# Kernel optimization log

Hardware: AMD Instinct MI355X
Metric: run time of the kernel (lower is better)

Reference implementation:

```python
import math
import jax, jax.numpy as jnp
import numpy as np

D_MODEL = 768
N_HEADS = 12
D_K = 64
D_V = 64
LN_EPS = 1e-5


def setup_inputs() -> dict:
    key = jax.random.key(0)
    ks = jax.random.split(key, 12)
    B, S = 4, 2048
    Q = jax.random.normal(ks[0], (B, S, D_MODEL), dtype=jnp.float32)
    K = jax.random.normal(ks[1], (B, S, D_MODEL), dtype=jnp.float32)
    V = jax.random.normal(ks[2], (B, S, D_MODEL), dtype=jnp.float32)
    attn_mask = jax.random.randint(ks[3], (B, S, S), 0, 2).astype(bool)
    sc = 1.0 / math.sqrt(D_MODEL)
    WQ = jax.random.normal(ks[4], (D_MODEL, N_HEADS * D_K), dtype=jnp.float32) * sc
    WK = jax.random.normal(ks[5], (D_MODEL, N_HEADS * D_K), dtype=jnp.float32) * sc
    WV = jax.random.normal(ks[6], (D_MODEL, N_HEADS * D_V), dtype=jnp.float32) * sc
    Wfc = jax.random.normal(ks[7], (N_HEADS * D_V, D_MODEL), dtype=jnp.float32) * sc
    bQ = jnp.zeros((N_HEADS * D_K,), jnp.float32)
    bK = jnp.zeros((N_HEADS * D_K,), jnp.float32)
    bV = jnp.zeros((N_HEADS * D_V,), jnp.float32)
    bfc = jnp.zeros((D_MODEL,), jnp.float32)
    gamma = jnp.ones((D_MODEL,), jnp.float32)
    beta = jnp.zeros((D_MODEL,), jnp.float32)
    return {"Q": Q, "K": K, "V": V, "attn_mask": attn_mask,
            "WQ": WQ, "bQ": bQ, "WK": WK, "bK": bK, "WV": WV, "bV": bV,
            "Wfc": Wfc, "bfc": bfc, "gamma": gamma, "beta": beta}


def reference(Q, K, V, attn_mask, WQ, bQ, WK, bK, WV, bV, Wfc, bfc, gamma, beta):
    B, S, _ = Q.shape
    # projections -> [B, H, S, d]
    q = (Q @ WQ + bQ).reshape(B, S, N_HEADS, D_K).transpose(0, 2, 1, 3)
    k = (K @ WK + bK).reshape(B, S, N_HEADS, D_K).transpose(0, 2, 1, 3)
    v = (V @ WV + bV).reshape(B, S, N_HEADS, D_V).transpose(0, 2, 1, 3)
    # manual scaled dot-product attention with masked_fill(-1e9)
    scores = jnp.einsum('bhqd,bhkd->bhqk', q, k) / math.sqrt(D_K)
    scores = jnp.where(attn_mask[:, None, :, :], jnp.float32(-1e9), scores)
    attn = jax.nn.softmax(scores, axis=-1)
    context = jnp.einsum('bhqk,bhkd->bhqd', attn, v)
    context = context.transpose(0, 2, 1, 3).reshape(B, S, N_HEADS * D_V)
    out = context @ Wfc + bfc + Q  # residual is Q
    # LayerNorm over d_model
    mu = jnp.mean(out, axis=-1, keepdims=True)
    var = jnp.mean((out - mu) ** 2, axis=-1, keepdims=True)
    return (out - mu) * jax.lax.rsqrt(var + LN_EPS) * gamma + beta
```

## Files before the change

### kernel.cpp

```cpp
#include <hip/hip_runtime.h>
#include <stdint.h>

#define DM   768
#define HEADS 12
#define DK    64
#define SEQ  2048
#define BATCH  4

typedef __bf16 bf16_t;
typedef __bf16 bf16x8 __attribute__((ext_vector_type(8)));
typedef __bf16 bf16x4 __attribute__((ext_vector_type(4)));
typedef float  f32x4  __attribute__((ext_vector_type(4)));
typedef float  f32x16 __attribute__((ext_vector_type(16)));
typedef unsigned u32x4 __attribute__((ext_vector_type(4)));

#define LOG2E 1.44269504f
#define MASKVAL (-1.442695e9f)

#define OFF_FLAG 0
#define OFF_MASK 256
#define SZ_MASK  (BATCH*SEQ*(SEQ/32)*4)
#define OFF_WT   (OFF_MASK + SZ_MASK)
#define SZ_WT1   (DM*DM*2)
#define OFF_XB   (OFF_WT + 4*SZ_WT1)
#define SZ_X     (BATCH*SEQ*DM*2)
#define OFF_QP   (OFF_XB + 3*SZ_X)
#define SZ_PROJ  (BATCH*HEADS*SEQ*DK*2)
#define OFF_KP   (OFF_QP + SZ_PROJ)
#define OFF_VT   (OFF_KP + SZ_PROJ)

__device__ __forceinline__ void gload_lds16(const bf16_t* g, bf16_t* l) {
    __builtin_amdgcn_global_load_lds((const __attribute__((address_space(1))) unsigned int*)g,
                                     (__attribute__((address_space(3))) unsigned int*)l, 16, 0, 0);
}

__device__ __forceinline__ unsigned pack2(float lo, float hi) {
    union { bf16_t b[2]; unsigned u; } x;
    x.b[0] = (bf16_t)lo; x.b[1] = (bf16_t)hi;
    return x.u;
}

__global__ void detect_mask_kernel(const unsigned char* __restrict__ m, int* flag) {
    int u = threadIdx.x;
    int any = m[4*u+1] | m[4*u+2] | m[4*u+3];
    unsigned long long b = __ballot(any != 0);
    if (u == 0) *flag = (b == 0ULL) ? 1 : 0;
}

__global__ void pack_mask_kernel(const void* __restrict__ mraw, const int* __restrict__ flag,
                                 unsigned int* __restrict__ words) {
    const unsigned int total = BATCH*SEQ*SEQ;
    const int is32 = *flag;
    const int* mi = (const int*)mraw;
    const unsigned char* mb = (const unsigned char*)mraw;
    unsigned int stride = gridDim.x * blockDim.x;
    unsigned int lane = threadIdx.x & 63u;
    for (unsigned int e = blockIdx.x * blockDim.x + threadIdx.x; e < total; e += stride) {
        int v = is32 ? (mi[e] != 0) : (mb[e] != 0);
        unsigned long long bal = __ballot(v);
        if ((lane & 31u) == 0u)
            words[e >> 5] = (unsigned int)(bal >> ((lane >> 5) * 32u));
    }
}

__global__ void wt_cvt_kernel(const float* __restrict__ W0, const float* __restrict__ W1,
                              const float* __restrict__ W2, const float* __restrict__ W3,
                              bf16_t* __restrict__ dst) {
    const float* W = blockIdx.z == 0 ? W0 : blockIdx.z == 1 ? W1 : blockIdx.z == 2 ? W2 : W3;
    bf16_t* out = dst + (size_t)blockIdx.z * DM * DM;
    __shared__ float tile[64][65];
    int w = threadIdx.x >> 6, u = threadIdx.x & 63;
    int kb = blockIdx.x * 64, nb = blockIdx.y * 64;
    #pragma unroll
    for (int i = 0; i < 16; i++)
        tile[w + 4*i][u] = W[(size_t)(kb + w + 4*i)*DM + nb + u];
    __syncthreads();
    #pragma unroll
    for (int i = 0; i < 16; i++)
        out[(size_t)(nb + w + 4*i)*DM + kb + u] = (bf16_t)tile[u][w + 4*i];
}

__global__ void xcvt_kernel(const float* __restrict__ Q, const float* __restrict__ K,
                            const float* __restrict__ V, bf16_t* __restrict__ XB) {
    int z = blockIdx.y;
    const float* src = z == 0 ? Q : z == 1 ? K : V;
    bf16_t* dst = XB + (size_t)z * BATCH*SEQ*DM;
    size_t i = ((size_t)blockIdx.x * blockDim.x + threadIdx.x) * 8;
    float4 a = *(const float4*)(src + i);
    float4 b = *(const float4*)(src + i + 4);
    bf16x8 o;
    o[0]=(bf16_t)a.x; o[1]=(bf16_t)a.y; o[2]=(bf16_t)a.z; o[3]=(bf16_t)a.w;
    o[4]=(bf16_t)b.x; o[5]=(bf16_t)b.y; o[6]=(bf16_t)b.z; o[7]=(bf16_t)b.w;
    *(bf16x8*)(dst + i) = o;
}

__device__ __forceinline__ void mm_mainloop(const bf16_t* __restrict__ Aptr,
                                            const bf16_t* __restrict__ Bptr,
                                            bf16_t* As, bf16_t* Bs,
                                            f32x4 acc[4][4], int bm, int bn) {
    int tid = threadIdx.x, w = tid >> 6, u = tid & 63, c = u & 15, g = u >> 4;
    int wr = w >> 1, wc = w & 1;
    for (int k0 = 0; k0 < DM; k0 += 64) {
        #pragma unroll
        for (int i = 0; i < 4; i++) {
            int q = i*256 + tid;
            int row = q >> 3, col8 = q & 7;
            gload_lds16(Aptr + (size_t)(bm*128 + row)*DM + k0 + col8*8, As + (i*256 + w*64)*8);
            gload_lds16(Bptr + (size_t)(bn*128 + row)*DM + k0 + col8*8, Bs + (i*256 + w*64)*8);
        }
        __syncthreads();
        #pragma unroll
        for (int kk = 0; kk < 2; kk++) {
            bf16x8 a[4], bfr[4];
            #pragma unroll
            for (int mi = 0; mi < 4; mi++)
                a[mi] = *(const bf16x8*)(As + (wr*64 + mi*16 + c)*64 + kk*32 + g*8);
            #pragma unroll
            for (int ni = 0; ni < 4; ni++)
                bfr[ni] = *(const bf16x8*)(Bs + (wc*64 + ni*16 + c)*64 + kk*32 + g*8);
            #pragma unroll
            for (int mi = 0; mi < 4; mi++)
                #pragma unroll
                for (int ni = 0; ni < 4; ni++)
                    acc[mi][ni] = __builtin_amdgcn_mfma_f32_16x16x32_bf16(a[mi], bfr[ni], acc[mi][ni], 0, 0, 0);
        }
        __syncthreads();
    }
}

__global__ __launch_bounds__(256) void proj128_kernel(
        const bf16_t* __restrict__ XB, const bf16_t* __restrict__ WT,
        const float* __restrict__ bQ, const float* __restrict__ bK, const float* __restrict__ bV,
        bf16_t* __restrict__ QP, bf16_t* __restrict__ KP, bf16_t* __restrict__ VT) {
    int z = blockIdx.z;
    const bf16_t* Aptr = XB + (size_t)z * BATCH*SEQ*DM;
    const bf16_t* Bptr = WT + (size_t)z * DM * DM;
    const float* bias = z == 0 ? bQ : z == 1 ? bK : bV;
    float scale = (z == 0) ? 0.125f * LOG2E : 1.0f;
    __shared__ __align__(16) bf16_t As[128*64], Bs[128*64];
    int tid = threadIdx.x, w = tid >> 6, u = tid & 63, c = u & 15, g = u >> 4;
    int wr = w >> 1, wc = w & 1;
    int bm = blockIdx.x, bn = blockIdx.y;
    f32x4 zero = {0.f,0.f,0.f,0.f};
    f32x4 acc[4][4] = {{zero,zero,zero,zero},{zero,zero,zero,zero},
                       {zero,zero,zero,zero},{zero,zero,zero,zero}};
    mm_mainloop(Aptr, Bptr, As, Bs, acc, bm, bn);
    int h = bn*2 + wc;
    #pragma unroll
    for (int ni = 0; ni < 4; ni++) {
        int d = ni*16 + c;
        float bv = bias[h*64 + d];
        if (z < 2) {
            bf16_t* dst = (z == 0) ? QP : KP;
            #pragma unroll
            for (int mi = 0; mi < 4; mi++)
                #pragma unroll
                for (int j = 0; j < 4; j++) {
                    int r = bm*128 + wr*64 + mi*16 + 4*g + j;
                    int bidx = r >> 11, s = r & 2047;
                    dst[(((size_t)bidx*HEADS + h)*SEQ + s)*DK + d] = (bf16_t)((acc[mi][ni][j] + bv)*scale);
                }
        } else {
            #pragma unroll
            for (int mi = 0; mi < 4; mi++) {
                bf16x4 pk;
                #pragma unroll
                for (int j = 0; j < 4; j++) pk[j] = (bf16_t)(acc[mi][ni][j] + bv);
                int r0 = bm*128 + wr*64 + mi*16 + 4*g;
                int bidx = r0 >> 11, s0 = r0 & 2047;
                *(bf16x4*)(VT + (((size_t)bidx*HEADS + h)*DK + d)*SEQ + s0) = pk;
            }
        }
    }
}

__global__ __launch_bounds__(256) void out128_kernel(
        const bf16_t* __restrict__ CTX, const bf16_t* __restrict__ WfcT,
        const float* __restrict__ bfc, const float* __restrict__ Qres, float* __restrict__ out) {
    __shared__ __align__(16) bf16_t As[128*64], Bs[128*64];
    int tid = threadIdx.x, w = tid >> 6, u = tid & 63, c = u & 15, g = u >> 4;
    int wr = w >> 1, wc = w & 1;
    int bm = blockIdx.x, bn = blockIdx.y;
    f32x4 zero = {0.f,0.f,0.f,0.f};
    f32x4 acc[4][4] = {{zero,zero,zero,zero},{zero,zero,zero,zero},
                       {zero,zero,zero,zero},{zero,zero,zero,zero}};
    mm_mainloop(CTX, WfcT, As, Bs, acc, bm, bn);
    #pragma unroll
    for (int ni = 0; ni < 4; ni++) {
        int n = bn*128 + wc*64 + ni*16 + c;
        float bv = bfc[n];
        #pragma unroll
        for (int mi = 0; mi < 4; mi++)
            #pragma unroll
            for (int j = 0; j < 4; j++) {
                int r = bm*128 + wr*64 + mi*16 + 4*g + j;
                out[(size_t)r*DM + n] = acc[mi][ni][j] + bv + Qres[(size_t)r*DM + n];
            }
    }
}

__global__ __launch_bounds__(256) void attn_kernel(
        const bf16_t* __restrict__ QP, const bf16_t* __restrict__ KP, const bf16_t* __restrict__ VT,
        const unsigned int* __restrict__ maskw, bf16_t* __restrict__ CTX) {
    __shared__ __align__(16) bf16_t kbuf[2][64*64];
    __shared__ __align__(16) bf16_t vbuf[2][64*64];
    int tid = threadIdx.x, w = tid >> 6, u = tid & 63;
    int qc = u & 31, hi = u >> 5;
    int b = blockIdx.z, h = blockIdx.y;
    int qg = blockIdx.x * 128 + w * 32 + qc;
    size_t bh = (size_t)(b * HEADS + h);
    const bf16_t* qp = QP + bh * SEQ * DK;
    const bf16_t* kp = KP + bh * SEQ * DK;
    const bf16_t* vt = VT + bh * DK * SEQ;
    const unsigned int* mwq = maskw + ((size_t)b * SEQ + qg) * (SEQ/32);

    bf16x8 qf[4];
    #pragma unroll
    for (int t = 0; t < 4; t++)
        qf[t] = *(const bf16x8*)(qp + (size_t)qg*DK + 16*t + 8*hi);

    int sr = tid >> 3, scc = tid & 7;

    f32x16 zz = {0,0,0,0,0,0,0,0,0,0,0,0,0,0,0,0};
    f32x16 acc0 = zz, acc1 = zz;
    float mrun = -3e38f, lsum = 0.f;

    #pragma unroll
    for (int i = 0; i < 2; i++) {
        int r = i*32 + sr;
        int gc = (scc ^ (r & 7)) << 3;
        gload_lds16(kp + (size_t)r*DK + gc,       &kbuf[0][0] + i*2048 + tid*8);
        gload_lds16(vt + (size_t)r*SEQ + 0 + gc,  &vbuf[0][0] + i*2048 + tid*8);
    }
    __syncthreads();

    for (int kt = 0; kt < SEQ/64; kt++) {
        int kb = kt * 64;
        int cur = kt & 1;
        if (kt + 1 < SEQ/64) {
            int nkb = kb + 64;
            #pragma unroll
            for (int i = 0; i < 2; i++) {
                int r = i*32 + sr;
                int gc = (scc ^ (r & 7)) << 3;
                gload_lds16(kp + (size_t)(nkb + r)*DK + gc, &kbuf[cur^1][0] + i*2048 + tid*8);
                gload_lds16(vt + (size_t)r*SEQ + nkb + gc,  &vbuf[cur^1][0] + i*2048 + tid*8);
            }
        }
        const bf16_t* kl = &kbuf[cur][0];
        const bf16_t* vl = &vbuf[cur][0];
        uint2 mv = *(const uint2*)(mwq + (kb >> 5));

        f32x16 s0 = zz, s1 = zz;
        __builtin_amdgcn_s_setprio(1);
        #pragma unroll
        for (int t = 0; t < 4; t++) {
            int col = (16*t + 8*hi);
            int r0 = qc, r1 = 32 + qc;
            bf16x8 k0 = *(const bf16x8*)(kl + r0*64 + (col ^ ((r0 & 7) << 3)));
            bf16x8 k1 = *(const bf16x8*)(kl + r1*64 + (col ^ ((r1 & 7) << 3)));
            s0 = __builtin_amdgcn_mfma_f32_32x32x16_bf16(k0, qf[t], s0, 0, 0, 0);
            s1 = __builtin_amdgcn_mfma_f32_32x32x16_bf16(k1, qf[t], s1, 0, 0, 0);
        }
        __builtin_amdgcn_s_setprio(0);

        #pragma unroll
        for (int r = 0; r < 16; r++) {
            int bit = (r & 3) + 8*(r >> 2) + 4*hi;
            if ((mv.x >> bit) & 1u) s0[r] = MASKVAL;
            if ((mv.y >> bit) & 1u) s1[r] = MASKVAL;
        }
        float tm[16];
        #pragma unroll
        for (int r = 0; r < 16; r++) tm[r] = fmaxf(s0[r], s1[r]);
        #pragma unroll
        for (int st = 8; st > 0; st >>= 1)
            #pragma unroll
            for (int r = 0; r < st; r++) tm[r] = fmaxf(tm[r], tm[r + st]);
        float rmax = fmaxf(tm[0], __shfl_xor(tm[0], 32));
        float mn = fmaxf(mrun, rmax);
        float alpha = exp2f(mrun - mn);
        mrun = mn;
        #pragma unroll
        for (int r = 0; r < 16; r++) {
            s0[r] = exp2f(s0[r] - mn);
            s1[r] = exp2f(s1[r] - mn);
        }
        float ts[16];
        #pragma unroll
        for (int r = 0; r < 16; r++) ts[r] = s0[r] + s1[r];
        #pragma unroll
        for (int st = 8; st > 0; st >>= 1)
            #pragma unroll
            for (int r = 0; r < st; r++) ts[r] = ts[r] + ts[r + st];
        float rsum = ts[0] + __shfl_xor(ts[0], 32);
        lsum = lsum * alpha + rsum;
        #pragma unroll
        for (int r = 0; r < 16; r++) { acc0[r] *= alpha; acc1[r] *= alpha; }

        bf16x8 pa[4];
        {
            union { u32x4 uv; bf16x8 bv; } cv;
            unsigned x0, y0, x1, y1;
            x0 = pack2(s0[0], s0[1]); y0 = pack2(s0[4], s0[5]);
            asm volatile("v_permlane32_swap_b32 %0, %1" : "+v"(x0), "+v"(y0));
            x1 = pack2(s0[2], s0[3]); y1 = pack2(s0[6], s0[7]);
            asm volatile("v_permlane32_swap_b32 %0, %1" : "+v"(x1), "+v"(y1));
            cv.uv[0]=x0; cv.uv[1]=x1; cv.uv[2]=y0; cv.uv[3]=y1; pa[0]=cv.bv;
            x0 = pack2(s0[8], s0[9]);  y0 = pack2(s0[12], s0[13]);
            asm volatile("v_permlane32_swap_b32 %0, %1" : "+v"(x0), "+v"(y0));
            x1 = pack2(s0[10], s0[11]); y1 = pack2(s0[14], s0[15]);
            asm volatile("v_permlane32_swap_b32 %0, %1" : "+v"(x1), "+v"(y1));
            cv.uv[0]=x0; cv.uv[1]=x1; cv.uv[2]=y0; cv.uv[3]=y1; pa[1]=cv.bv;
            x0 = pack2(s1[0], s1[1]); y0 = pack2(s1[4], s1[5]);
            asm volatile("v_permlane32_swap_b32 %0, %1" : "+v"(x0), "+v"(y0));
            x1 = pack2(s1[2], s1[3]); y1 = pack2(s1[6], s1[7]);
            asm volatile("v_permlane32_swap_b32 %0, %1" : "+v"(x1), "+v"(y1));
            cv.uv[0]=x0; cv.uv[1]=x1; cv.uv[2]=y0; cv.uv[3]=y1; pa[2]=cv.bv;
            x0 = pack2(s1[8], s1[9]);  y0 = pack2(s1[12], s1[13]);
            asm volatile("v_permlane32_swap_b32 %0, %1" : "+v"(x0), "+v"(y0));
            x1 = pack2(s1[10], s1[11]); y1 = pack2(s1[14], s1[15]);
            asm volatile("v_permlane32_swap_b32 %0, %1" : "+v"(x1), "+v"(y1));
            cv.uv[0]=x0; cv.uv[1]=x1; cv.uv[2]=y0; cv.uv[3]=y1; pa[3]=cv.bv;
        }

        __builtin_amdgcn_s_setprio(1);
        #pragma unroll
        for (int ks = 0; ks < 4; ks++) {
            int col = 16*ks + 8*hi;
            int r0 = qc, r1 = 32 + qc;
            bf16x8 v0 = *(const bf16x8*)(vl + r0*64 + (col ^ ((r0 & 7) << 3)));
            bf16x8 v1 = *(const bf16x8*)(vl + r1*64 + (col ^ ((r1 & 7) << 3)));
            acc0 = __builtin_amdgcn_mfma_f32_32x32x16_bf16(v0, pa[ks], acc0, 0, 0, 0);
            acc1 = __builtin_amdgcn_mfma_f32_32x32x16_bf16(v1, pa[ks], acc1, 0, 0, 0);
        }
        __builtin_amdgcn_s_setprio(0);

        __syncthreads();
    }

    float inv = 1.0f / lsum;
    size_t obase = ((size_t)(b * SEQ) + qg) * DM + h * DK;
    #pragma unroll
    for (int gr = 0; gr < 4; gr++) {
        bf16x4 o0, o1;
        #pragma unroll
        for (int jj = 0; jj < 4; jj++) {
            o0[jj] = (bf16_t)(acc0[4*gr + jj] * inv);
            o1[jj] = (bf16_t)(acc1[4*gr + jj] * inv);
        }
        *(bf16x4*)(CTX + obase + gr*8 + hi*4)      = o0;
        *(bf16x4*)(CTX + obase + 32 + gr*8 + hi*4) = o1;
    }
}

__global__ __launch_bounds__(256) void ln_kernel(float* __restrict__ out,
        const float* __restrict__ gamma, const float* __restrict__ beta) {
    int w = threadIdx.x >> 6, u = threadIdx.x & 63;
    size_t row = (size_t)blockIdx.x * 4 + w;
    float x[12];
    float s = 0.f;
    #pragma unroll
    for (int i = 0; i < 12; i++) { x[i] = out[row*DM + i*64 + u]; s += x[i]; }
    #pragma unroll
    for (int d = 1; d < 64; d <<= 1) s += __shfl_xor(s, d);
    float mu = s * (1.0f/768.0f);
    float v = 0.f;
    #pragma unroll
    for (int i = 0; i < 12; i++) { float t = x[i] - mu; v += t*t; }
    #pragma unroll
    for (int d = 1; d < 64; d <<= 1) v += __shfl_xor(v, d);
    float rstd = rsqrtf(v * (1.0f/768.0f) + 1e-5f);
    #pragma unroll
    for (int i = 0; i < 12; i++)
        out[row*DM + i*64 + u] = (x[i] - mu) * rstd * gamma[i*64 + u] + beta[i*64 + u];
}

extern "C" void kernel_launch(void* const* d_in, const int* in_sizes, int n_in,
                              void* d_out, int out_size, void* d_ws, size_t ws_size,
                              hipStream_t stream) {
    const float* Q    = (const float*)d_in[0];
    const float* K    = (const float*)d_in[1];
    const float* V    = (const float*)d_in[2];
    const void*  mask = d_in[3];
    const float* WQ   = (const float*)d_in[4];
    const float* bQ   = (const float*)d_in[5];
    const float* WK   = (const float*)d_in[6];
    const float* bK   = (const float*)d_in[7];
    const float* WV   = (const float*)d_in[8];
    const float* bV   = (const float*)d_in[9];
    const float* Wfc  = (const float*)d_in[10];
    const float* bfc  = (const float*)d_in[11];
    const float* gam  = (const float*)d_in[12];
    const float* bet  = (const float*)d_in[13];
    float* out = (float*)d_out;
    char* ws = (char*)d_ws;

    int* flag            = (int*)(ws + OFF_FLAG);
    unsigned int* maskw  = (unsigned int*)(ws + OFF_MASK);
    bf16_t* WT           = (bf16_t*)(ws + OFF_WT);
    bf16_t* XB           = (bf16_t*)(ws + OFF_XB);
    bf16_t* QP           = (bf16_t*)(ws + OFF_QP);
    bf16_t* KP           = (bf16_t*)(ws + OFF_KP);
    bf16_t* VT           = (bf16_t*)(ws + OFF_VT);
    bf16_t* CTX          = XB;

    detect_mask_kernel<<<1, 64, 0, stream>>>((const unsigned char*)mask, flag);
    pack_mask_kernel<<<2048, 256, 0, stream>>>(mask, flag, maskw);
    xcvt_kernel<<<dim3(3072, 3), 256, 0, stream>>>(Q, K, V, XB);
    wt_cvt_kernel<<<dim3(12, 12, 4), 256, 0, stream>>>(WQ, WK, WV, Wfc, WT);
    proj128_kernel<<<dim3(64, 6, 3), 256, 0, stream>>>(XB, WT, bQ, bK, bV, QP, KP, VT);
    attn_kernel<<<dim3(SEQ/128, HEADS, BATCH), 256, 0, stream>>>(QP, KP, VT, maskw, CTX);
    out128_kernel<<<dim3(64, 6), 256, 0, stream>>>(CTX, WT + (size_t)3*DM*DM, bfc, Q, out);
    ln_kernel<<<2048, 256, 0, stream>>>(out, gam, bet);
}
```

Baseline: 448.7 us.

## Defer softmax rescaling with threshold and apply mask via LDS lookup table

```diff
diff --git a/kernel.cpp b/kernel.cpp
--- a/kernel.cpp
+++ b/kernel.cpp
@@ -16,6 +16,7 @@
 
 #define LOG2E 1.44269504f
 #define MASKVAL (-1.442695e9f)
+#define DEFER_THR 8.0f
 
 #define OFF_FLAG 0
 #define OFF_MASK 256
@@ -204,6 +205,7 @@
         const unsigned int* __restrict__ maskw, bf16_t* __restrict__ CTX) {
     __shared__ __align__(16) bf16_t kbuf[2][64*64];
     __shared__ __align__(16) bf16_t vbuf[2][64*64];
+    __shared__ __align__(16) float lut4[64];
     int tid = threadIdx.x, w = tid >> 6, u = tid & 63;
     int qc = u & 31, hi = u >> 5;
     int b = blockIdx.z, h = blockIdx.y;
@@ -214,6 +216,8 @@
     const bf16_t* vt = VT + bh * DK * SEQ;
     const unsigned int* mwq = maskw + ((size_t)b * SEQ + qg) * (SEQ/32);
 
+    if (tid < 64) lut4[tid] = (((tid >> 2) >> (tid & 3)) & 1) ? MASKVAL : 0.f;
+
     bf16x8 qf[4];
     #pragma unroll
     for (int t = 0; t < 4; t++)
@@ -232,12 +236,15 @@
         gload_lds16(kp + (size_t)r*DK + gc,       &kbuf[0][0] + i*2048 + tid*8);
         gload_lds16(vt + (size_t)r*SEQ + 0 + gc,  &vbuf[0][0] + i*2048 + tid*8);
     }
+    uint2 mv = *(const uint2*)(mwq);
     __syncthreads();
 
     for (int kt = 0; kt < SEQ/64; kt++) {
         int kb = kt * 64;
         int cur = kt & 1;
+        uint2 mv_next;
         if (kt + 1 < SEQ/64) {
+            mv_next = *(const uint2*)(mwq + ((kb + 64) >> 5));
             int nkb = kb + 64;
             #pragma unroll
             for (int i = 0; i < 2; i++) {
@@ -249,7 +256,13 @@
         }
         const bf16_t* kl = &kbuf[cur][0];
         const bf16_t* vl = &vbuf[cur][0];
-        uint2 mv = *(const uint2*)(mwq + (kb >> 5));
+
+        f32x4 am0[4], am1[4];
+        #pragma unroll
+        for (int j = 0; j < 4; j++) {
+            am0[j] = *(const f32x4*)&lut4[((mv.x >> (8*j + 4*hi)) & 0xFu) * 4];
+            am1[j] = *(const f32x4*)&lut4[((mv.y >> (8*j + 4*hi)) & 0xFu) * 4];
+        }
 
         f32x16 s0 = zz, s1 = zz;
         __builtin_amdgcn_s_setprio(1);
@@ -265,38 +278,45 @@
         __builtin_amdgcn_s_setprio(0);
 
         #pragma unroll
+        for (int j = 0; j < 4; j++)
+            #pragma unroll
+            for (int i = 0; i < 4; i++) {
+                s0[4*j + i] += am0[j][i];
+                s1[4*j + i] += am1[j][i];
+            }
+
+        float tmx[16];
+        #pragma unroll
+        for (int r = 0; r < 16; r++) tmx[r] = fmaxf(s0[r], s1[r]);
+        #pragma unroll
+        for (int st = 8; st > 0; st >>= 1)
+            #pragma unroll
+            for (int r = 0; r < st; r++) tmx[r] = fmaxf(tmx[r], tmx[r + st]);
+        float tm = tmx[0];
+
+        if (!__all(tm <= mrun + DEFER_THR)) {
+            float rmax = fmaxf(tm, __shfl_xor(tm, 32));
+            float mn = fmaxf(mrun, rmax);
+            float alpha = __builtin_amdgcn_exp2f(mrun - mn);
+            mrun = mn;
+            lsum *= alpha;
+            acc0 *= alpha;
+            acc1 *= alpha;
+        }
+
+        #pragma unroll
         for (int r = 0; r < 16; r++) {
-            int bit = (r & 3) + 8*(r >> 2) + 4*hi;
-            if ((mv.x >> bit) & 1u) s0[r] = MASKVAL;
-            if ((mv.y >> bit) & 1u) s1[r] = MASKVAL;
-        }
-        float tm[16];
-        #pragma unroll
-        for (int r = 0; r < 16; r++) tm[r] = fmaxf(s0[r], s1[r]);
+            s0[r] = __builtin_amdgcn_exp2f(s0[r] - mrun);
+            s1[r] = __builtin_amdgcn_exp2f(s1[r] - mrun);
+        }
+        float sm[16];
+        #pragma unroll
+        for (int r = 0; r < 16; r++) sm[r] = s0[r] + s1[r];
         #pragma unroll
         for (int st = 8; st > 0; st >>= 1)
             #pragma unroll
-            for (int r = 0; r < st; r++) tm[r] = fmaxf(tm[r], tm[r + st]);
-        float rmax = fmaxf(tm[0], __shfl_xor(tm[0], 32));
-        float mn = fmaxf(mrun, rmax);
-        float alpha = exp2f(mrun - mn);
-        mrun = mn;
-        #pragma unroll
-        for (int r = 0; r < 16; r++) {
-            s0[r] = exp2f(s0[r] - mn);
-            s1[r] = exp2f(s1[r] - mn);
-        }
-        float ts[16];
-        #pragma unroll
-        for (int r = 0; r < 16; r++) ts[r] = s0[r] + s1[r];
-        #pragma unroll
-        for (int st = 8; st > 0; st >>= 1)
-            #pragma unroll
-            for (int r = 0; r < st; r++) ts[r] = ts[r] + ts[r + st];
-        float rsum = ts[0] + __shfl_xor(ts[0], 32);
-        lsum = lsum * alpha + rsum;
-        #pragma unroll
-        for (int r = 0; r < 16; r++) { acc0[r] *= alpha; acc1[r] *= alpha; }
+            for (int r = 0; r < st; r++) sm[r] = sm[r] + sm[r + st];
+        lsum += sm[0] + __shfl_xor(sm[0], 32);
 
         bf16x8 pa[4];
         {
@@ -337,6 +357,7 @@
         __builtin_amdgcn_s_setprio(0);
 
         __syncthreads();
+        mv = mv_next;
     }
 
     float inv = 1.0f / lsum;
```

After: 400.7 us. -10.7%, faster.
